# Kernel tuning notes

Hardware: AMD Instinct MI355X
Metric: run time of the kernel (lower is better)

## Reference

```python
import jax, jax.numpy as jnp
import numpy as np

N_NODES = 100000
N_EDGES = 3200000
F_IN, F_HID, F_OUT = 512, 128, 32


def setup_inputs() -> dict:
    key = jax.random.key(0)
    ks = jax.random.split(key, 8)
    x = jax.random.normal(ks[0], (N_NODES, F_IN), dtype=jnp.float32)
    edge_row = jax.random.randint(ks[1], (N_EDGES,), 0, N_NODES, dtype=jnp.int32)
    edge_col = jax.random.randint(ks[2], (N_EDGES,), 0, N_NODES, dtype=jnp.int32)
    edge_val = jax.random.uniform(ks[3], (N_EDGES,), dtype=jnp.float32)
    W1 = jax.random.normal(ks[4], (F_IN, F_HID), dtype=jnp.float32) / np.sqrt(F_IN)
    b1 = jnp.zeros((F_HID,), dtype=jnp.float32)
    W2 = jax.random.normal(ks[5], (F_HID, F_OUT), dtype=jnp.float32) / np.sqrt(F_HID)
    b2 = jnp.zeros((F_OUT,), dtype=jnp.float32)
    return {"x": x, "edge_row": edge_row, "edge_col": edge_col,
            "edge_val": edge_val, "W1": W1, "b1": b1, "W2": W2, "b2": b2}


def _spmm(edge_row, edge_col, edge_val, dense):
    # out[r] = sum_{e: row[e]==r} val[e] * dense[col[e]]  (COO SpMM)
    gathered = dense[edge_col] * edge_val[:, None]  # [E, F]
    return jax.ops.segment_sum(gathered, edge_row, num_segments=N_NODES)


def reference(x, edge_row, edge_col, edge_val, W1, b1, W2, b2):
    # GraphConvolution 1: support = x@W1; out = A @ support + b1
    h = _spmm(edge_row, edge_col, edge_val, x @ W1) + b1
    h = jax.nn.relu(h)
    # GraphConvolution 2
    logits = _spmm(edge_row, edge_col, edge_val, h @ W2) + b2
    return jax.nn.log_softmax(logits, axis=1)
```

## Files before the change

kernel.cpp:

```cpp
#include <hip/hip_runtime.h>


#define NN 100000
#define NE 3200000
#define FIN 512
#define FHID 128
#define FOUT 32
#define BROWS 64
#define NBUCK 1563
#define NPART 256
#define CHUNK 12800
#define TOT (NBUCK * NPART)
#define NSCAN1 391
#define GG1 ((NN + 127) / 128)
#define EBCAP 2560

typedef __attribute__((ext_vector_type(8))) short bf16x8;
typedef __attribute__((ext_vector_type(4))) float f32x4;

static __device__ __forceinline__ unsigned short f2bf(float f) {
    unsigned u = __float_as_uint(f);
    unsigned r = (u + 0x7FFFu + ((u >> 16) & 1u)) >> 16;
    return (unsigned short)r;
}
static __device__ __forceinline__ float bf2f(unsigned short u) {
    return __uint_as_float(((unsigned)u) << 16);
}
static __device__ __forceinline__ float bflo(unsigned u) {
    return __uint_as_float(u << 16);
}
static __device__ __forceinline__ float bfhi(unsigned u) {
    return __uint_as_float(u & 0xffff0000u);
}
static __device__ __forceinline__ bf16x8 pack8(float4 u, float4 v) {
    bf16x8 r;
    r[0] = (short)f2bf(u.x); r[1] = (short)f2bf(u.y);
    r[2] = (short)f2bf(u.z); r[3] = (short)f2bf(u.w);
    r[4] = (short)f2bf(v.x); r[5] = (short)f2bf(v.y);
    r[6] = (short)f2bf(v.z); r[7] = (short)f2bf(v.w);
    return r;
}

__global__ __launch_bounds__(256) void fused_prep_hist(const float* __restrict__ W1,
                                                       unsigned short* __restrict__ W1t,
                                                       const int* __restrict__ erow,
                                                       int* __restrict__ cntG) {
    if (blockIdx.x < NPART) {
        __shared__ int c[NBUCK];
        const int t = threadIdx.x;
        const int w = blockIdx.x;
        for (int i = t; i < NBUCK; i += 256) c[i] = 0;
        __syncthreads();
        const int e0 = w * CHUNK;
        const int e1 = min(e0 + CHUNK, NE);
        for (int e = e0 + t; e < e1; e += 256) atomicAdd(&c[erow[e] >> 6], 1);
        __syncthreads();
        for (int i = t; i < NBUCK; i += 256) cntG[w * NBUCK + i] = c[i];
    } else {
        int t = (blockIdx.x - NPART) * 256 + threadIdx.x;
        int j = t & 7;
        int c = t >> 3;
        int l = c & 63;
        int ks = (c >> 6) & 15;
        int nt = c >> 10;
        int n = nt * 16 + (l & 15);
        int k = ks * 32 + ((l >> 4) << 3) + j;
        W1t[(size_t)c * 8 + j] = f2bf(W1[k * FHID + n]);
    }
}

__global__ __launch_bounds__(256) void scan1_kernel(const int* __restrict__ cntG,
                                                    int* __restrict__ off,
                                                    int* __restrict__ partials) {
    __shared__ int s[256];
    int t = threadIdx.x;
    int i0 = blockIdx.x * 1024 + t * 4;
    int v[4];
#pragma unroll
    for (int j = 0; j < 4; ++j) {
        int i = i0 + j;
        v[j] = (i < TOT) ? cntG[(i & (NPART - 1)) * NBUCK + (i >> 8)] : 0;
    }
    int lsum = v[0] + v[1] + v[2] + v[3];
    s[t] = lsum;
    __syncthreads();
    for (int o = 1; o < 256; o <<= 1) {
        int xv = (t >= o) ? s[t - o] : 0;
        __syncthreads();
        s[t] += xv;
        __syncthreads();
    }
    if (t == 255) partials[blockIdx.x] = s[255];
    int run = s[t] - lsum;
#pragma unroll
    for (int j = 0; j < 4; ++j) {
        if (i0 + j < TOT) off[i0 + j] = run;
        run += v[j];
    }
}

__global__ __launch_bounds__(512) void scan2_kernel(int* partials) {
    __shared__ int s[512];
    int t = threadIdx.x;
    int v = (t < NSCAN1) ? partials[t] : 0;
    s[t] = v;
    __syncthreads();
    for (int o = 1; o < 512; o <<= 1) {
        int xv = (t >= o) ? s[t - o] : 0;
        __syncthreads();
        s[t] += xv;
        __syncthreads();
    }
    if (t < NSCAN1) partials[t] = s[t] - v;
}

__global__ __launch_bounds__(256) void scan3_kernel(int* __restrict__ off,
                                                    const int* __restrict__ partials) {
    int add = partials[blockIdx.x];
    int i0 = blockIdx.x * 1024 + threadIdx.x * 4;
#pragma unroll
    for (int j = 0; j < 4; ++j)
        if (i0 + j < TOT) off[i0 + j] += add;
}

__global__ __launch_bounds__(256) void fused_scatter_gemm1(
    const int* __restrict__ erow, const int* __restrict__ ecol,
    const float* __restrict__ eval, const int* __restrict__ off,
    int2* __restrict__ bcolval,
    const float* __restrict__ x, const unsigned short* __restrict__ W1t,
    unsigned short* __restrict__ outd) {
    if (blockIdx.x < NPART) {
        __shared__ int pos[NBUCK];
        const int t = threadIdx.x;
        const int w = blockIdx.x;
        for (int b = t; b < NBUCK; b += 256) pos[b] = off[b * NPART + w];
        __syncthreads();
        const int e0 = w * CHUNK;
        const int e1 = min(e0 + CHUNK, NE);
        for (int e = e0 + t; e < e1; e += 256) {
            int r = erow[e];
            int idx = atomicAdd(&pos[r >> 6], 1);
            bcolval[idx] = make_int2(ecol[e] | ((r & 63) << 20), __float_as_int(eval[e]));
        }
    } else {
        const int tid = threadIdx.x;
        const int lane = tid & 63;
        const int w = tid >> 6;
        const int quad = lane >> 4;
        const int m = lane & 15;
        const int row0 = (blockIdx.x - NPART) * 128 + w * 32;

        int rA = row0 + m;
        int rB = row0 + 16 + m;
        rA = rA < NN ? rA : NN - 1;
        rB = rB < NN ? rB : NN - 1;
        const float* pA = x + (size_t)rA * FIN + quad * 8;
        const float* pB = x + (size_t)rB * FIN + quad * 8;

        f32x4 acc[2][8];
#pragma unroll
        for (int i = 0; i < 2; ++i)
#pragma unroll
            for (int nt = 0; nt < 8; ++nt) acc[i][nt] = (f32x4){0.f, 0.f, 0.f, 0.f};

        float4 a0 = *(const float4*)pA;
        float4 a1 = *(const float4*)(pA + 4);
        float4 b0 = *(const float4*)pB;
        float4 b1 = *(const float4*)(pB + 4);

        for (int ks = 0; ks < 16; ++ks) {
            const int kn = (ks + 1) & 15;
            float4 na0 = *(const float4*)(pA + kn * 32);
            float4 na1 = *(const float4*)(pA + kn * 32 + 4);
            float4 nb0 = *(const float4*)(pB + kn * 32);
            float4 nb1 = *(const float4*)(pB + kn * 32 + 4);

            bf16x8 fA = pack8(a0, a1);
            bf16x8 fB = pack8(b0, b1);
            bf16x8 bb[8];
#pragma unroll
            for (int nt = 0; nt < 8; ++nt)
                bb[nt] = *(const bf16x8*)(W1t + ((size_t)((nt * 16 + ks) * 64 + lane)) * 8);
#pragma unroll
            for (int nt = 0; nt < 8; ++nt) {
                acc[0][nt] = __builtin_amdgcn_mfma_f32_16x16x32_bf16(fA, bb[nt], acc[0][nt], 0, 0, 0);
                acc[1][nt] = __builtin_amdgcn_mfma_f32_16x16x32_bf16(fB, bb[nt], acc[1][nt], 0, 0, 0);
            }
            a0 = na0; a1 = na1; b0 = nb0; b1 = nb1;
        }

#pragma unroll
        for (int i = 0; i < 2; ++i)
#pragma unroll
            for (int nt = 0; nt < 8; ++nt) {
                int col = nt * 16 + m;
#pragma unroll
                for (int r = 0; r < 4; ++r) {
                    int row = row0 + i * 16 + quad * 4 + r;
                    if (row < NN) outd[(size_t)row * FHID + col] = f2bf(acc[i][nt][r]);
                }
            }
    }
}

__global__ __launch_bounds__(256) void bucket_to_csr(const int* __restrict__ off,
                                                     const int2* __restrict__ bcolval,
                                                     int* __restrict__ rowptr,
                                                     int2* __restrict__ epack) {
    __shared__ int cnt[BROWS];
    __shared__ int pos[BROWS];
    __shared__ int s[BROWS];
    __shared__ int2 eb[EBCAP];
    const int b = blockIdx.x;
    const int t = threadIdx.x;
    const int s0 = off[b * NPART];
    const int send = (b == NBUCK - 1) ? NE : off[(b + 1) * NPART];
    const int n = send - s0;
    const bool fits = (n <= EBCAP);
    if (t < BROWS) cnt[t] = 0;
    __syncthreads();
    int2 myv[10];
    if (fits) {
#pragma unroll
        for (int ii = 0; ii < 10; ++ii) {
            int i = t + ii * 256;
            int2 v = make_int2(0, 0);
            if (i < n) {
                v = bcolval[s0 + i];
                atomicAdd(&cnt[((unsigned)v.x) >> 20], 1);
            }
            myv[ii] = v;
        }
    } else {
        for (int i = t; i < n; i += 256)
            atomicAdd(&cnt[((unsigned)bcolval[s0 + i].x) >> 20], 1);
    }
    __syncthreads();
    int myc = (t < BROWS) ? cnt[t] : 0;
    if (t < BROWS) s[t] = myc;
    __syncthreads();
    for (int o = 1; o < BROWS; o <<= 1) {
        int xv = (t >= o && t < BROWS) ? s[t - o] : 0;
        __syncthreads();
        if (t < BROWS) s[t] += xv;
        __syncthreads();
    }
    if (t < BROWS) {
        int excl = s[t] - myc;
        pos[t] = excl;
        int row = b * BROWS + t;
        if (row < NN) rowptr[row] = s0 + excl;
    }
    if (b == 0 && t == 0) rowptr[NN] = NE;
    __syncthreads();
    if (fits) {
#pragma unroll
        for (int ii = 0; ii < 10; ++ii) {
            int i = t + ii * 256;
            if (i < n) {
                int2 v = myv[ii];
                int p = atomicAdd(&pos[((unsigned)v.x) >> 20], 1);
                eb[p] = make_int2(v.x & 0xFFFFF, v.y);
            }
        }
        __syncthreads();
        for (int i = t; i < n; i += 256) epack[s0 + i] = eb[i];
    } else {
        for (int i = t; i < n; i += 256) {
            int2 v = bcolval[s0 + i];
            int p = atomicAdd(&pos[((unsigned)v.x) >> 20], 1);
            epack[s0 + p] = make_int2(v.x & 0xFFFFF, v.y);
        }
    }
}

__global__ __launch_bounds__(256) void spmm1_kernel(const int* __restrict__ rowptr,
                                                    const int2* __restrict__ epack,
                                                    const unsigned short* __restrict__ dense,
                                                    const float* __restrict__ b1,
                                                    unsigned short* __restrict__ h) {
    const int lane = threadIdx.x & 63;
    const int row = blockIdx.x * 4 + (threadIdx.x >> 6);
    const int start = __builtin_amdgcn_readfirstlane(rowptr[row]);
    const int cnt = __builtin_amdgcn_readfirstlane(rowptr[row + 1]) - start;
    const int sl16 = lane & 15;
    const unsigned* d32 = (const unsigned*)dense;
    float acc0 = 0.f, acc1 = 0.f;

    int j = 0;
    for (; j + 32 <= cnt; j += 32) {
        int2 p0 = epack[start + j + sl16];
        int2 p1 = epack[start + j + 16 + sl16];
        unsigned d[32];
#pragma unroll
        for (int k = 0; k < 16; ++k) {
            int c = __builtin_amdgcn_readlane(p0.x, k);
            d[k] = d32[((size_t)c << 6) + lane];
        }
#pragma unroll
        for (int k = 0; k < 16; ++k) {
            int c = __builtin_amdgcn_readlane(p1.x, k);
            d[16 + k] = d32[((size_t)c << 6) + lane];
        }
#pragma unroll
        for (int k = 0; k < 16; ++k) {
            float v = __int_as_float(__builtin_amdgcn_readlane(p0.y, k));
            acc0 = fmaf(v, bflo(d[k]), acc0);
            acc1 = fmaf(v, bfhi(d[k]), acc1);
        }
#pragma unroll
        for (int k = 0; k < 16; ++k) {
            float v = __int_as_float(__builtin_amdgcn_readlane(p1.y, k));
            acc0 = fmaf(v, bflo(d[16 + k]), acc0);
            acc1 = fmaf(v, bfhi(d[16 + k]), acc1);
        }
    }
    if (j + 16 <= cnt) {
        int2 p = epack[start + j + sl16];
        unsigned d[16];
#pragma unroll
        for (int k = 0; k < 16; ++k) {
            int c = __builtin_amdgcn_readlane(p.x, k);
            d[k] = d32[((size_t)c << 6) + lane];
        }
#pragma unroll
        for (int k = 0; k < 16; ++k) {
            float v = __int_as_float(__builtin_amdgcn_readlane(p.y, k));
            acc0 = fmaf(v, bflo(d[k]), acc0);
            acc1 = fmaf(v, bfhi(d[k]), acc1);
        }
        j += 16;
    }
    const int rem = cnt - j;
    if (rem > 0) {
        int idx = j + (sl16 < rem ? sl16 : rem - 1);
        int2 p = epack[start + idx];
        unsigned d[16];
#pragma unroll
        for (int k = 0; k < 16; ++k) {
            int c = __builtin_amdgcn_readlane(p.x, k);
            c = (k < rem) ? c : 0;
            d[k] = d32[((size_t)c << 6) + lane];
        }
#pragma unroll
        for (int k = 0; k < 16; ++k) {
            float v = (k < rem) ? __int_as_float(__builtin_amdgcn_readlane(p.y, k)) : 0.f;
            acc0 = fmaf(v, bflo(d[k]), acc0);
            acc1 = fmaf(v, bfhi(d[k]), acc1);
        }
    }
    float2 bb = *(const float2*)(b1 + lane * 2);
    unsigned r0 = f2bf(fmaxf(acc0 + bb.x, 0.f));
    unsigned r1 = f2bf(fmaxf(acc1 + bb.y, 0.f));
    *((unsigned*)(h + (size_t)row * FHID) + lane) = r0 | (r1 << 16);
}

__global__ __launch_bounds__(256) void gemm2_kernel(const unsigned short* __restrict__ h,
                                                    const float* __restrict__ W2,
                                                    unsigned short* __restrict__ out) {
    __shared__ float hs[64][129];
    const int tid = threadIdx.x;
    const int lane = tid & 63;
    const int cg = __builtin_amdgcn_readfirstlane(tid >> 6);
    const int row0 = blockIdx.x * 64;
    const int row = row0 + lane;

    float acc[8];
#pragma unroll
    for (int c = 0; c < 8; ++c) acc[c] = 0.f;

#pragma unroll
    for (int j = 0; j < 8; ++j) {
        int f4 = tid + j * 256;
        int r = f4 >> 5;
        int kq = f4 & 31;
        ushort4 v = make_ushort4(0, 0, 0, 0);
        if (row0 + r < NN) v = *(const ushort4*)(h + (size_t)(row0 + r) * FHID + kq * 4);
        hs[r][kq * 4 + 0] = bf2f(v.x);
        hs[r][kq * 4 + 1] = bf2f(v.y);
        hs[r][kq * 4 + 2] = bf2f(v.z);
        hs[r][kq * 4 + 3] = bf2f(v.w);
    }
    __syncthreads();
#pragma unroll 4
    for (int k = 0; k < FHID; ++k) {
        float a = hs[lane][k];
        const float* wrow = W2 + k * FOUT + cg * 8;
#pragma unroll
        for (int c = 0; c < 8; ++c) acc[c] += a * wrow[c];
    }
    if (row < NN) {
        uint4 st;
        st.x = (unsigned)f2bf(acc[0]) | ((unsigned)f2bf(acc[1]) << 16);
        st.y = (unsigned)f2bf(acc[2]) | ((unsigned)f2bf(acc[3]) << 16);
        st.z = (unsigned)f2bf(acc[4]) | ((unsigned)f2bf(acc[5]) << 16);
        st.w = (unsigned)f2bf(acc[6]) | ((unsigned)f2bf(acc[7]) << 16);
        *(uint4*)(out + (size_t)row * FOUT + cg * 8) = st;
    }
}

__global__ __launch_bounds__(256) void spmm2_kernel(const int* __restrict__ rowptr,
                                                    const int2* __restrict__ epack,
                                                    const unsigned short* __restrict__ dense,
                                                    const float* __restrict__ b2,
                                                    float* __restrict__ out) {
    const int lane = threadIdx.x & 63;
    const int row = blockIdx.x * 4 + (threadIdx.x >> 6);
    const int start = __builtin_amdgcn_readfirstlane(rowptr[row]);
    const int cnt = __builtin_amdgcn_readfirstlane(rowptr[row + 1]) - start;
    const int quad = lane >> 4;
    const int sl16 = lane & 15;
    const unsigned* d32 = (const unsigned*)dense;
    float acc0 = 0.f, acc1 = 0.f;

    int j = 0;
    for (; j + 16 <= cnt; j += 16) {
        int2 p = epack[start + j + sl16];
        unsigned d[4];
        float vv[4];
#pragma unroll
        for (int k = 0; k < 16; ++k) {
            int c = __builtin_amdgcn_readlane(p.x, k);
            int v = __builtin_amdgcn_readlane(p.y, k);
            if ((k >> 2) == quad) {
                d[k & 3] = d32[((size_t)c << 4) + sl16];
                vv[k & 3] = __int_as_float(v);
            }
        }
#pragma unroll
        for (int k = 0; k < 4; ++k) {
            acc0 = fmaf(vv[k], bflo(d[k]), acc0);
            acc1 = fmaf(vv[k], bfhi(d[k]), acc1);
        }
    }
    const int rem = cnt - j;
    if (rem > 0) {
        int idx = j + (sl16 < rem ? sl16 : rem - 1);
        int2 p = epack[start + idx];
        unsigned d[4];
        float vv[4];
#pragma unroll
        for (int k = 0; k < 4; ++k) { d[k] = 0; vv[k] = 0.f; }
#pragma unroll
        for (int k = 0; k < 16; ++k) {
            int c = __builtin_amdgcn_readlane(p.x, k);
            int v = __builtin_amdgcn_readlane(p.y, k);
            c = (k < rem) ? c : 0;
            if ((k >> 2) == quad) {
                d[k & 3] = d32[((size_t)c << 4) + sl16];
                vv[k & 3] = (k < rem) ? __int_as_float(v) : 0.f;
            }
        }
#pragma unroll
        for (int k = 0; k < 4; ++k) {
            acc0 = fmaf(vv[k], bflo(d[k]), acc0);
            acc1 = fmaf(vv[k], bfhi(d[k]), acc1);
        }
    }
    acc0 += __shfl_xor(acc0, 16, 64);
    acc0 += __shfl_xor(acc0, 32, 64);
    acc1 += __shfl_xor(acc1, 16, 64);
    acc1 += __shfl_xor(acc1, 32, 64);
    float2 bb = *(const float2*)(b2 + sl16 * 2);
    acc0 += bb.x;
    acc1 += bb.y;
    float m = fmaxf(acc0, acc1);
#pragma unroll
    for (int mask = 8; mask >= 1; mask >>= 1) m = fmaxf(m, __shfl_xor(m, mask, 64));
    float ssum = expf(acc0 - m) + expf(acc1 - m);
#pragma unroll
    for (int mask = 8; mask >= 1; mask >>= 1) ssum += __shfl_xor(ssum, mask, 64);
    float lse = m + logf(ssum);
    if (lane < 16) {
        float2 st = make_float2(acc0 - lse, acc1 - lse);
        *(float2*)(out + (size_t)row * FOUT + sl16 * 2) = st;
    }
}

extern "C" void kernel_launch(void* const* d_in, const int* in_sizes, int n_in,
                              void* d_out, int out_size, void* d_ws, size_t ws_size,
                              hipStream_t stream) {
    const float* x = (const float*)d_in[0];
    const int* erow = (const int*)d_in[1];
    const int* ecol = (const int*)d_in[2];
    const float* eval = (const float*)d_in[3];
    const float* W1 = (const float*)d_in[4];
    const float* b1 = (const float*)d_in[5];
    const float* W2 = (const float*)d_in[6];
    const float* b2 = (const float*)d_in[7];
    float* out = (float*)d_out;

    char* ws = (char*)d_ws;
    size_t off_b = 0;
    auto walloc = [&](size_t bytes) -> void* {
        void* p = ws + off_b;
        off_b = (off_b + bytes + 255) & ~(size_t)255;
        return p;
    };
    int2* epack = (int2*)walloc((size_t)NE * 8);
    int* rowptr = (int*)walloc((size_t)(NN + 1) * 4);
    int* cntG = (int*)walloc((size_t)TOT * 4);
    int* off = (int*)walloc((size_t)TOT * 4);
    int* partials = (int*)walloc(4096);
    unsigned short* W1t = (unsigned short*)walloc((size_t)FHID * FIN * 2);
    int2* bcolval = (int2*)walloc((size_t)NE * 8);
    unsigned short* support1 = (unsigned short*)walloc((size_t)NN * FHID * 2);
    unsigned short* h = (unsigned short*)walloc((size_t)NN * FHID * 2);
    unsigned short* support2 = support1;

    fused_prep_hist<<<NPART + 256, 256, 0, stream>>>(W1, W1t, erow, cntG);
    scan1_kernel<<<NSCAN1, 256, 0, stream>>>(cntG, off, partials);
    scan2_kernel<<<1, 512, 0, stream>>>(partials);
    scan3_kernel<<<NSCAN1, 256, 0, stream>>>(off, partials);
    fused_scatter_gemm1<<<NPART + GG1, 256, 0, stream>>>(erow, ecol, eval, off,
                                                         bcolval, x, W1t, support1);
    bucket_to_csr<<<NBUCK, 256, 0, stream>>>(off, bcolval, rowptr, epack);
    spmm1_kernel<<<NN / 4, 256, 0, stream>>>(rowptr, epack, support1, b1, h);
    gemm2_kernel<<<(NN + 63) / 64, 256, 0, stream>>>(h, W2, support2);
    spmm2_kernel<<<NN / 4, 256, 0, stream>>>(rowptr, epack, support2, b2, out);
}
```

Baseline: 644.6 us.

## Stage edge scatter through LDS local bucket sort and split GEMM1 out

The edge scatter becomes its own 512-thread kernel. Each partition counts its edges per bucket in LDS, runs a local prefix scan, sorts its records into LDS, then writes them out as contiguous runs per bucket. Before, each edge was written to a random global location. The GEMM1 path, which used to share a launch with the scatter, is now a separate kernel launched after bucket_to_csr. This should coalesce the scatter writes, but it gives up the overlap between scatter and GEMM. The new scatter kernel uses about 140KB of LDS per block, so only one block fits per CU.

```diff
diff --git a/kernel.cpp b/kernel.cpp
--- a/kernel.cpp
+++ b/kernel.cpp
@@ -9,11 +9,11 @@
 #define BROWS 64
 #define NBUCK 1563
 #define NPART 256
-#define CHUNK 12800
+#define CHUNK 12500
 #define TOT (NBUCK * NPART)
 #define NSCAN1 391
-#define GG1 ((NN + 127) / 128)
 #define EBCAP 2560
+#define EPT 25
 
 typedef __attribute__((ext_vector_type(8))) short bf16x8;
 typedef __attribute__((ext_vector_type(4))) float f32x4;
@@ -123,83 +123,78 @@
         if (i0 + j < TOT) off[i0 + j] += add;
 }
 
-__global__ __launch_bounds__(256) void fused_scatter_gemm1(
-    const int* __restrict__ erow, const int* __restrict__ ecol,
-    const float* __restrict__ eval, const int* __restrict__ off,
-    int2* __restrict__ bcolval,
-    const float* __restrict__ x, const unsigned short* __restrict__ W1t,
-    unsigned short* __restrict__ outd) {
-    if (blockIdx.x < NPART) {
-        __shared__ int pos[NBUCK];
-        const int t = threadIdx.x;
-        const int w = blockIdx.x;
-        for (int b = t; b < NBUCK; b += 256) pos[b] = off[b * NPART + w];
-        __syncthreads();
-        const int e0 = w * CHUNK;
-        const int e1 = min(e0 + CHUNK, NE);
-        for (int e = e0 + t; e < e1; e += 256) {
+__global__ __launch_bounds__(512) void scatter_part(const int* __restrict__ erow,
+                                                    const int* __restrict__ ecol,
+                                                    const float* __restrict__ eval,
+                                                    const int* __restrict__ off,
+                                                    int2* __restrict__ bcolval) {
+    __shared__ int2 eb2[CHUNK];
+    __shared__ unsigned short bkt2[CHUNK];
+    __shared__ int cnt[NBUCK];
+    __shared__ int pos[NBUCK];
+    __shared__ int s[512];
+    const int t = threadIdx.x;
+    const int w = blockIdx.x;
+    const int e0 = w * CHUNK;
+
+    for (int i = t; i < NBUCK; i += 512) cnt[i] = 0;
+    __syncthreads();
+
+    int myb[EPT];
+    int2 myrec[EPT];
+#pragma unroll
+    for (int ii = 0; ii < EPT; ++ii) {
+        int i = t + ii * 512;
+        myb[ii] = -1;
+        if (i < CHUNK) {
+            int e = e0 + i;
             int r = erow[e];
-            int idx = atomicAdd(&pos[r >> 6], 1);
-            bcolval[idx] = make_int2(ecol[e] | ((r & 63) << 20), __float_as_int(eval[e]));
-        }
-    } else {
-        const int tid = threadIdx.x;
-        const int lane = tid & 63;
-        const int w = tid >> 6;
-        const int quad = lane >> 4;
-        const int m = lane & 15;
-        const int row0 = (blockIdx.x - NPART) * 128 + w * 32;
-
-        int rA = row0 + m;
-        int rB = row0 + 16 + m;
-        rA = rA < NN ? rA : NN - 1;
-        rB = rB < NN ? rB : NN - 1;
-        const float* pA = x + (size_t)rA * FIN + quad * 8;
-        const float* pB = x + (size_t)rB * FIN + quad * 8;
-
-        f32x4 acc[2][8];
-#pragma unroll
-        for (int i = 0; i < 2; ++i)
-#pragma unroll
-            for (int nt = 0; nt < 8; ++nt) acc[i][nt] = (f32x4){0.f, 0.f, 0.f, 0.f};
-
-        float4 a0 = *(const float4*)pA;
-        float4 a1 = *(const float4*)(pA + 4);
-        float4 b0 = *(const float4*)pB;
-        float4 b1 = *(const float4*)(pB + 4);
-
-        for (int ks = 0; ks < 16; ++ks) {
-            const int kn = (ks + 1) & 15;
-            float4 na0 = *(const float4*)(pA + kn * 32);
-            float4 na1 = *(const float4*)(pA + kn * 32 + 4);
-            float4 nb0 = *(const float4*)(pB + kn * 32);
-            float4 nb1 = *(const float4*)(pB + kn * 32 + 4);
-
-            bf16x8 fA = pack8(a0, a1);
-            bf16x8 fB = pack8(b0, b1);
-            bf16x8 bb[8];
-#pragma unroll
-            for (int nt = 0; nt < 8; ++nt)
-                bb[nt] = *(const bf16x8*)(W1t + ((size_t)((nt * 16 + ks) * 64 + lane)) * 8);
-#pragma unroll
-            for (int nt = 0; nt < 8; ++nt) {
-                acc[0][nt] = __builtin_amdgcn_mfma_f32_16x16x32_bf16(fA, bb[nt], acc[0][nt], 0, 0, 0);
-                acc[1][nt] = __builtin_amdgcn_mfma_f32_16x16x32_bf16(fB, bb[nt], acc[1][nt], 0, 0, 0);
-            }
-            a0 = na0; a1 = na1; b0 = nb0; b1 = nb1;
-        }
-
-#pragma unroll
-        for (int i = 0; i < 2; ++i)
-#pragma unroll
-            for (int nt = 0; nt < 8; ++nt) {
-                int col = nt * 16 + m;
-#pragma unroll
-                for (int r = 0; r < 4; ++r) {
-                    int row = row0 + i * 16 + quad * 4 + r;
-                    if (row < NN) outd[(size_t)row * FHID + col] = f2bf(acc[i][nt][r]);
-                }
-            }
+            int b = r >> 6;
+            myb[ii] = b;
+            myrec[ii] = make_int2(ecol[e] | ((r & 63) << 20), __float_as_int(eval[e]));
+            atomicAdd(&cnt[b], 1);
+        }
+    }
+    __syncthreads();
+
+    int base = t * 4;
+    int v[4];
+#pragma unroll
+    for (int j = 0; j < 4; ++j) v[j] = (base + j < NBUCK) ? cnt[base + j] : 0;
+    int lsum = v[0] + v[1] + v[2] + v[3];
+    s[t] = lsum;
+    __syncthreads();
+    for (int o = 1; o < 512; o <<= 1) {
+        int xv = (t >= o) ? s[t - o] : 0;
+        __syncthreads();
+        s[t] += xv;
+        __syncthreads();
+    }
+    int run = s[t] - lsum;
+#pragma unroll
+    for (int j = 0; j < 4; ++j) {
+        if (base + j < NBUCK) cnt[base + j] = run;
+        run += v[j];
+    }
+    __syncthreads();
+    for (int i = t; i < NBUCK; i += 512) pos[i] = cnt[i];
+    __syncthreads();
+
+#pragma unroll
+    for (int ii = 0; ii < EPT; ++ii) {
+        if (myb[ii] >= 0) {
+            int ld = atomicAdd(&pos[myb[ii]], 1);
+            eb2[ld] = myrec[ii];
+            bkt2[ld] = (unsigned short)myb[ii];
+        }
+    }
+    __syncthreads();
+
+    for (int i = t; i < CHUNK; i += 512) {
+        int2 rec = eb2[i];
+        int b = bkt2[i];
+        int dest = off[b * NPART + w] + (i - cnt[b]);
+        bcolval[dest] = rec;
     }
 }
 
@@ -272,6 +267,68 @@
             epack[s0 + p] = make_int2(v.x & 0xFFFFF, v.y);
         }
     }
+}
+
+__global__ __launch_bounds__(256) void gemm1_mfma(const float* __restrict__ x,
+                                                  const unsigned short* __restrict__ W1t,
+                                                  unsigned short* __restrict__ out) {
+    const int tid = threadIdx.x;
+    const int lane = tid & 63;
+    const int w = tid >> 6;
+    const int quad = lane >> 4;
+    const int m = lane & 15;
+    const int row0 = blockIdx.x * 128 + w * 32;
+
+    int rA = row0 + m;
+    int rB = row0 + 16 + m;
+    rA = rA < NN ? rA : NN - 1;
+    rB = rB < NN ? rB : NN - 1;
+    const float* pA = x + (size_t)rA * FIN + quad * 8;
+    const float* pB = x + (size_t)rB * FIN + quad * 8;
+
+    f32x4 acc[2][8];
+#pragma unroll
+    for (int i = 0; i < 2; ++i)
+#pragma unroll
+        for (int nt = 0; nt < 8; ++nt) acc[i][nt] = (f32x4){0.f, 0.f, 0.f, 0.f};
+
+    float4 a0 = *(const float4*)pA;
+    float4 a1 = *(const float4*)(pA + 4);
+    float4 b0 = *(const float4*)pB;
+    float4 b1 = *(const float4*)(pB + 4);
+
+    for (int ks = 0; ks < 16; ++ks) {
+        const int kn = (ks + 1) & 15;
+        float4 na0 = *(const float4*)(pA + kn * 32);
+        float4 na1 = *(const float4*)(pA + kn * 32 + 4);
+        float4 nb0 = *(const float4*)(pB + kn * 32);
+        float4 nb1 = *(const float4*)(pB + kn * 32 + 4);
+
+        bf16x8 fA = pack8(a0, a1);
+        bf16x8 fB = pack8(b0, b1);
+        bf16x8 bb[8];
+#pragma unroll
+        for (int nt = 0; nt < 8; ++nt)
+            bb[nt] = *(const bf16x8*)(W1t + ((size_t)((nt * 16 + ks) * 64 + lane)) * 8);
+#pragma unroll
+        for (int nt = 0; nt < 8; ++nt) {
+            acc[0][nt] = __builtin_amdgcn_mfma_f32_16x16x32_bf16(fA, bb[nt], acc[0][nt], 0, 0, 0);
+            acc[1][nt] = __builtin_amdgcn_mfma_f32_16x16x32_bf16(fB, bb[nt], acc[1][nt], 0, 0, 0);
+        }
+        a0 = na0; a1 = na1; b0 = nb0; b1 = nb1;
+    }
+
+#pragma unroll
+    for (int i = 0; i < 2; ++i)
+#pragma unroll
+        for (int nt = 0; nt < 8; ++nt) {
+            int col = nt * 16 + m;
+#pragma unroll
+            for (int r = 0; r < 4; ++r) {
+                int row = row0 + i * 16 + quad * 4 + r;
+                if (row < NN) out[(size_t)row * FHID + col] = f2bf(acc[i][nt][r]);
+            }
+        }
 }
 
 __global__ __launch_bounds__(256) void spmm1_kernel(const int* __restrict__ rowptr,
@@ -512,9 +569,9 @@
     scan1_kernel<<<NSCAN1, 256, 0, stream>>>(cntG, off, partials);
     scan2_kernel<<<1, 512, 0, stream>>>(partials);
     scan3_kernel<<<NSCAN1, 256, 0, stream>>>(off, partials);
-    fused_scatter_gemm1<<<NPART + GG1, 256, 0, stream>>>(erow, ecol, eval, off,
-                                                         bcolval, x, W1t, support1);
+    scatter_part<<<NPART, 512, 0, stream>>>(erow, ecol, eval, off, bcolval);
     bucket_to_csr<<<NBUCK, 256, 0, stream>>>(off, bcolval, rowptr, epack);
+    gemm1_mfma<<<(NN + 127) / 128, 256, 0, stream>>>(x, W1t, support1);
     spmm1_kernel<<<NN / 4, 256, 0, stream>>>(rowptr, epack, support1, b1, h);
     gemm2_kernel<<<(NN + 63) / 64, 256, 0, stream>>>(h, W2, support2);
     spmm2_kernel<<<NN / 4, 256, 0, stream>>>(rowptr, epack, support2, b2, out);
```

Result: faster. 606.4 us (-5.9%).
